# Kernel optimization log

Hardware: AMD Instinct MI355X
Metric: run time of the kernel (lower is better)

Reference implementation:

```python
import jax, jax.numpy as jnp
import numpy as np

N = 100000   # num nodes
E = 1600000  # num edges
F = 64       # node_feature_dim
H = 128      # hidden_dim
G = 64       # num graphs in batch
L = 3        # num_gnn_layers


def setup_inputs() -> dict:
    key = jax.random.key(0)
    ks = jax.random.split(key, 24)
    s = 0.05
    nrm = lambda k, shape: jax.random.normal(k, shape, jnp.float32) * s
    return dict(
        node_features=jax.random.normal(ks[0], (N, F), jnp.float32),
        edge_index=jax.random.randint(ks[1], (2, E), 0, N, dtype=jnp.int32),
        batch=jnp.sort(jax.random.randint(ks[2], (N,), 0, G, dtype=jnp.int32)),
        enc_w1=nrm(ks[3], (F, H)), enc_b1=jnp.zeros((H,), jnp.float32),
        enc_w2=nrm(ks[4], (H, H)), enc_b2=jnp.zeros((H,), jnp.float32),
        gcn_w=nrm(ks[5], (L, H, H)), gcn_b=jnp.zeros((L, H), jnp.float32),
        dec_w1=nrm(ks[6], (2 * H, H)), dec_b1=jnp.zeros((H,), jnp.float32),
        dec_w2=nrm(ks[7], (H, 64)), dec_b2=jnp.zeros((64,), jnp.float32),
        dec_w3=nrm(ks[8], (64, 3)), dec_b3=jnp.zeros((3,), jnp.float32),
        val_w1=nrm(ks[9], (2 * H, H)), val_b1=jnp.zeros((H,), jnp.float32),
        val_w2=nrm(ks[10], (H, 1)), val_b2=jnp.zeros((1,), jnp.float32),
    )


def _forward(node_features, edge_index, batch,
             enc_w1, enc_b1, enc_w2, enc_b2, gcn_w, gcn_b,
             dec_w1, dec_b1, dec_w2, dec_b2, dec_w3, dec_b3,
             val_w1, val_b1, val_w2, val_b2):
    n = node_features.shape[0]
    # node encoder (dropout is identity in eval)
    x = jax.nn.relu(node_features @ enc_w1 + enc_b1)
    x = x @ enc_w2 + enc_b2

    # GCN normalization with self-loops (PyG gcn_norm)
    loops = jnp.arange(n, dtype=edge_index.dtype)
    src = jnp.concatenate([edge_index[0], loops])
    dst = jnp.concatenate([edge_index[1], loops])
    deg = jax.ops.segment_sum(jnp.ones_like(src, jnp.float32), dst, num_segments=n)
    dinv = jax.lax.rsqrt(deg)  # deg >= 1 due to self-loops
    norm = (dinv[src] * dinv[dst])[:, None]  # [E+N, 1]

    for l in range(gcn_w.shape[0]):
        xw = x @ gcn_w[l]                      # [N, H]
        msg = xw[src] * norm                   # gather + scale
        agg = jax.ops.segment_sum(msg, dst, num_segments=n) + gcn_b[l]
        x = x + jax.nn.relu(agg)               # residual

    # global pools per graph
    graph_sum = jax.ops.segment_sum(x, batch, num_segments=G)
    counts = jax.ops.segment_sum(jnp.ones((n, 1), x.dtype), batch, num_segments=G)
    graph_mean = graph_sum / jnp.maximum(counts, 1.0)
    graph_max = jax.ops.segment_max(x, batch, num_segments=G)
    graph_repr = jnp.concatenate([graph_mean, graph_max], axis=1)  # [G, 2H]

    h = jax.nn.relu(graph_repr @ dec_w1 + dec_b1)
    h = jax.nn.relu(h @ dec_w2 + dec_b2)
    logits = h @ dec_w3 + dec_b3               # [G, 3]

    adaptation_prob = jax.nn.sigmoid(logits[:, 0])
    layer_priorities = jax.nn.softmax(logits[:, 1:2], axis=-1)
    urgency_score = jax.nn.sigmoid(logits[:, 2])

    v = jax.nn.relu(graph_repr @ val_w1 + val_b1)
    value_estimate = v @ val_w2 + val_b2       # [G, 1]
    return adaptation_prob, layer_priorities, urgency_score, value_estimate


def reference(node_features, edge_index, batch,
              enc_w1, enc_b1, enc_w2, enc_b2, gcn_w, gcn_b,
              dec_w1, dec_b1, dec_w2, dec_b2, dec_w3, dec_b3,
              val_w1, val_b1, val_w2, val_b2):
    return _forward(node_features, edge_index, batch,
                    enc_w1, enc_b1, enc_w2, enc_b2, gcn_w, gcn_b,
                    dec_w1, dec_b1, dec_w2, dec_b2, dec_w3, dec_b3,
                    val_w1, val_b1, val_w2, val_b2)
```

## Files before the change

kernel.cpp:

```cpp
#include <hip/hip_runtime.h>
#include <math.h>

constexpr int HD = 128;
constexpr int FD = 64;
constexpr int PCH = 32;
constexpr int BKT_SHIFT = 8;
constexpr int EPB = 8192;
constexpr float FP8_SCALE = 16.f;
constexpr float FP8_INV_SCALE = 1.f / 16.f;

typedef unsigned int uint;
typedef unsigned short ushort;
typedef unsigned char uchar;

using bf16x8 = __attribute__((ext_vector_type(8))) short;
using f32x4  = __attribute__((ext_vector_type(4))) float;

#if defined(__has_builtin)
#if __has_builtin(__builtin_amdgcn_cvt_pk_f32_fp8) && __has_builtin(__builtin_amdgcn_cvt_pk_fp8_f32)
#define HW_FP8 1
#endif
#endif

static __device__ inline ushort f2bf(float f) {
  uint u = __float_as_uint(f);
  return (ushort)((u + 0x7fffu + ((u >> 16) & 1u)) >> 16);
}
static __device__ inline float bf2f(ushort b) {
  return __uint_as_float((uint)b << 16);
}
static __device__ inline uint pack2bf(float a, float b) {
  return (uint)f2bf(a) | ((uint)f2bf(b) << 16);
}

static __device__ inline uchar enc_fp8_byte(float f) {
#ifdef HW_FP8
  return (uchar)(__builtin_amdgcn_cvt_pk_fp8_f32(f, f, 0, false) & 0xff);
#else
  float a = fabsf(f);
  uint s = (f < 0.f) ? 0x80u : 0u;
  if (!(a > 0.f)) return (uchar)s;
  a = fminf(a, 448.f);
  uint b = __float_as_uint(a);
  int e = (int)(b >> 23) - 127;
  if (e < -6) {
    int q = (int)rintf(a * 512.f);
    if (q <= 0) return (uchar)s;
    if (q >= 8) return (uchar)(s | 0x08u);
    return (uchar)(s | (uint)q);
  }
  uint r = b + 0x7ffffu + ((b >> 20) & 1u);
  uint m = (r >> 20) & 7u;
  int ee = (int)(r >> 23) - 127 + 7;
  if (ee <= 0) return (uchar)(s | 0x08u);
  if (ee > 15) return (uchar)(s | 0x7eu);
  return (uchar)(s | ((uint)ee << 3) | m);
#endif
}

static __device__ inline float dec_fp8_byte(uint em_s) {
  uint s = (em_s & 0x80u) << 24;
  uint em = em_s & 0x7fu;
  float v;
  if (em < 8) v = (float)em * (1.f / 512.f);
  else v = __uint_as_float((em + (120u << 3)) << 20);
  return __uint_as_float(__float_as_uint(v) | s);
}

static __device__ inline void dec_fp8x4(uint u, float* dst) {
#ifdef HW_FP8
  auto a = __builtin_amdgcn_cvt_pk_f32_fp8((int)u, false);
  auto b = __builtin_amdgcn_cvt_pk_f32_fp8((int)u, true);
  dst[0] = a[0]; dst[1] = a[1]; dst[2] = b[0]; dst[3] = b[1];
#else
  dst[0] = dec_fp8_byte(u & 0xffu);
  dst[1] = dec_fp8_byte((u >> 8) & 0xffu);
  dst[2] = dec_fp8_byte((u >> 16) & 0xffu);
  dst[3] = dec_fp8_byte(u >> 24);
#endif
}

__global__ void zero_int_kernel(int* __restrict__ p, int n) {
  int i = blockIdx.x * blockDim.x + threadIdx.x;
  if (i < n) p[i] = 0;
}

__global__ __launch_bounds__(256) void bucket_count_kernel(const int* __restrict__ dst,
    int* __restrict__ bucket_count, int e, int nbk) {
  __shared__ int hist[512];
  int t = threadIdx.x;
  for (int i = t; i < nbk; i += 256) hist[i] = 0;
  __syncthreads();
  int lo = blockIdx.x * EPB;
  int hi = lo + EPB; if (hi > e) hi = e;
  for (int i = lo + t; i < hi; i += 256) atomicAdd(&hist[dst[i] >> BKT_SHIFT], 1);
  __syncthreads();
  for (int i = t; i < nbk; i += 256) {
    int c = hist[i];
    if (c) atomicAdd(&bucket_count[i], c);
  }
}

__global__ __launch_bounds__(512) void bucket_scan_kernel(const int* __restrict__ bucket_count,
    int* __restrict__ bucket_base, int* __restrict__ bucket_cursor, int nbk) {
  __shared__ int sh[512];
  int t = threadIdx.x;
  int v = (t < nbk) ? bucket_count[t] : 0;
  sh[t] = v;
  __syncthreads();
  for (int d = 1; d < 512; d <<= 1) {
    int u = (t >= d) ? sh[t - d] : 0;
    __syncthreads();
    sh[t] += u;
    __syncthreads();
  }
  if (t < nbk) {
    int ex = sh[t] - v;
    bucket_base[t] = ex;
    bucket_cursor[t] = ex;
  }
  if (t == 511) bucket_base[nbk] = sh[511];
}

__global__ __launch_bounds__(256) void bucket_fill_kernel(const int* __restrict__ src,
    const int* __restrict__ dst, int* __restrict__ bucket_cursor,
    uint* __restrict__ pairs, int e, int nbk) {
  __shared__ int hist[512];
  int t = threadIdx.x;
  for (int i = t; i < nbk; i += 256) hist[i] = 0;
  __syncthreads();
  int lo = blockIdx.x * EPB;
  int hi = lo + EPB; if (hi > e) hi = e;
  for (int i = lo + t; i < hi; i += 256) atomicAdd(&hist[dst[i] >> BKT_SHIFT], 1);
  __syncthreads();
  for (int i = t; i < nbk; i += 256) {
    int c = hist[i];
    hist[i] = c ? atomicAdd(&bucket_cursor[i], c) : 0;
  }
  __syncthreads();
  for (int i = lo + t; i < hi; i += 256) {
    int s = src[i], d = dst[i];
    int pos = atomicAdd(&hist[d >> BKT_SHIFT], 1);
    pairs[pos] = ((uint)s << 8) | (uint)(d & 255);
  }
}

__global__ __launch_bounds__(256) void bucket_scatter_kernel(const uint* __restrict__ pairs,
    const int* __restrict__ bucket_base, int* __restrict__ offs,
    float* __restrict__ dinv, int* __restrict__ csr_src, int n, int nbk) {
  __shared__ int cnt[256];
  __shared__ int pre[256];
  int b = blockIdx.x, t = threadIdx.x;
  int node0 = b << BKT_SHIFT;
  bool valid_node = (node0 + t) < n;
  cnt[t] = 0;
  __syncthreads();
  int lo = bucket_base[b], hi = bucket_base[b + 1];
  for (int i = lo + t; i < hi; i += 256)
    atomicAdd(&cnt[pairs[i] & 255u], 1);
  __syncthreads();
  int v = cnt[t];
  pre[t] = v;
  __syncthreads();
  for (int d = 1; d < 256; d <<= 1) {
    int u = (t >= d) ? pre[t - d] : 0;
    __syncthreads();
    pre[t] += u;
    __syncthreads();
  }
  int off = lo + pre[t] - v;
  if (valid_node) {
    offs[node0 + t] = off;
    dinv[node0 + t] = rsqrtf((float)(v + 1));
  }
  __syncthreads();
  cnt[t] = off;
  __syncthreads();
  for (int i = lo + t; i < hi; i += 256) {
    uint pp = pairs[i];
    int pos = atomicAdd(&cnt[pp & 255u], 1);
    csr_src[pos] = (int)(pp >> 8);
  }
  if (b == 0 && t == 0) offs[n] = bucket_base[nbk];
}

__global__ void convert_wt_kernel(const float* __restrict__ W, ushort* __restrict__ wt,
                                  int KK) {
  int i = blockIdx.x * 256 + threadIdx.x;
  if (i < 128 * KK) {
    int c = i / KK, k = i - c * KK;
    wt[i] = f2bf(W[k * 128 + c]);
  }
}

template<typename TA, int K, bool BIAS, bool RELU, bool FP8OUT>
__global__ __launch_bounds__(256) void mfma_gemm_kernel(const TA* __restrict__ A,
    const ushort* __restrict__ Wt, const float* __restrict__ bias,
    void* __restrict__ Cout, const float* __restrict__ dinv, int M) {
  __shared__ ushort As[64 * K];
  __shared__ ushort Ws[128 * K];
  const int tid = threadIdx.x;
  const int r0 = blockIdx.x * 64;

  if constexpr (sizeof(TA) == 4) {
    constexpr int C4 = K / 4;
    const float4* A4 = (const float4*)A;
    #pragma unroll
    for (int i = tid; i < 64 * C4; i += 256) {
      int r = i / C4, c4 = i - r * C4;
      int row = r0 + r;
      float4 v = make_float4(0.f, 0.f, 0.f, 0.f);
      if (row < M) v = A4[(size_t)row * C4 + c4];
      ushort4 u;
      u.x = f2bf(v.x); u.y = f2bf(v.y); u.z = f2bf(v.z); u.w = f2bf(v.w);
      int elem = (r * K + c4 * 4) ^ ((r & 7) << 3);
      *(ushort4*)&As[elem] = u;
    }
  } else {
    constexpr int C8 = K / 8;
    const uint4* A4 = (const uint4*)A;
    #pragma unroll
    for (int i = tid; i < 64 * C8; i += 256) {
      int r = i / C8, c8 = i - r * C8;
      int row = r0 + r;
      uint4 v = make_uint4(0u, 0u, 0u, 0u);
      if (row < M) v = A4[(size_t)row * C8 + c8];
      int elem = (r * K + c8 * 8) ^ ((r & 7) << 3);
      *(uint4*)&As[elem] = v;
    }
  }
  {
    constexpr int C8 = K / 8;
    const uint4* W4 = (const uint4*)Wt;
    #pragma unroll
    for (int i = tid; i < 128 * C8; i += 256) {
      int c = i / C8, k8 = i - c * C8;
      uint4 v = W4[i];
      int elem = (c * K + k8 * 8) ^ ((c & 7) << 3);
      *(uint4*)&Ws[elem] = v;
    }
  }
  __syncthreads();

  const int l = tid & 63;
  const int wid = tid >> 6;
  const int lr = l & 15;
  const int lk = l >> 4;
  const int wr = wid * 16;
  f32x4 acc[8];
  #pragma unroll
  for (int cb = 0; cb < 8; ++cb) acc[cb] = (f32x4){0.f, 0.f, 0.f, 0.f};

  #pragma unroll
  for (int kc = 0; kc < K / 32; ++kc) {
    int ar = wr + lr;
    bf16x8 af = *(const bf16x8*)&As[(ar * K + kc * 32 + lk * 8) ^ ((ar & 7) << 3)];
    #pragma unroll
    for (int cb = 0; cb < 8; ++cb) {
      int col = cb * 16 + lr;
      bf16x8 bfr = *(const bf16x8*)&Ws[(col * K + kc * 32 + lk * 8) ^ ((col & 7) << 3)];
      acc[cb] = __builtin_amdgcn_mfma_f32_16x16x32_bf16(af, bfr, acc[cb], 0, 0, 0);
    }
  }

  if constexpr (FP8OUT) {
    uchar* C8p = (uchar*)Cout;
    float dv[4];
    #pragma unroll
    for (int j = 0; j < 4; ++j) {
      int row = r0 + wr + lk * 4 + j;
      dv[j] = (row < M) ? dinv[row] * FP8_SCALE : 0.f;
    }
    #pragma unroll
    for (int cb = 0; cb < 8; ++cb) {
      int col = cb * 16 + lr;
      #pragma unroll
      for (int j = 0; j < 4; ++j) {
        int row = r0 + wr + lk * 4 + j;
        if (row < M) {
          C8p[(size_t)row * 128 + col] = enc_fp8_byte(acc[cb][j] * dv[j]);
        }
      }
    }
  } else {
    ushort* Cb = (ushort*)Cout;
    #pragma unroll
    for (int cb = 0; cb < 8; ++cb) {
      int col = cb * 16 + lr;
      float bb = BIAS ? bias[col] : 0.f;
      #pragma unroll
      for (int j = 0; j < 4; ++j) {
        int row = r0 + wr + lk * 4 + j;
        if (row < M) {
          float o = acc[cb][j] + bb;
          if (RELU) o = fmaxf(o, 0.f);
          Cb[(size_t)row * 128 + col] = f2bf(o);
        }
      }
    }
  }
}

__global__ __launch_bounds__(256) void agg_update_kernel(
    const uchar* __restrict__ xws, ushort* __restrict__ x,
    const int* __restrict__ csr_src, const int* __restrict__ offs,
    const float* __restrict__ dinv, const float* __restrict__ bias, int n) {
  int node = blockIdx.x * 4 + (threadIdx.x >> 6);
  if (node >= n) return;
  int lane = threadIdx.x & 63;
  int grp = lane >> 4;
  int cl = lane & 15;
  const uint2* xw2 = (const uint2*)xws;
  float acc[8];
  #pragma unroll
  for (int k = 0; k < 8; ++k) acc[k] = 0.f;

  auto add_row = [&](uint2 v) {
    float f[4];
    dec_fp8x4(v.x, f);
    acc[0] += f[0]; acc[1] += f[1]; acc[2] += f[2]; acc[3] += f[3];
    dec_fp8x4(v.y, f);
    acc[4] += f[0]; acc[5] += f[1]; acc[6] += f[2]; acc[7] += f[3];
  };

  int beg = offs[node], end = offs[node + 1];
  int j = beg + grp;
  for (; j + 12 < end; j += 16) {
    int s0 = csr_src[j];
    int s1 = csr_src[j + 4];
    int s2 = csr_src[j + 8];
    int s3 = csr_src[j + 12];
    uint2 v0 = xw2[(size_t)s0 * 16 + cl];
    uint2 v1 = xw2[(size_t)s1 * 16 + cl];
    uint2 v2 = xw2[(size_t)s2 * 16 + cl];
    uint2 v3 = xw2[(size_t)s3 * 16 + cl];
    add_row(v0); add_row(v1); add_row(v2); add_row(v3);
  }
  for (; j + 4 < end; j += 8) {
    int s0 = csr_src[j];
    int s1 = csr_src[j + 4];
    uint2 v0 = xw2[(size_t)s0 * 16 + cl];
    uint2 v1 = xw2[(size_t)s1 * 16 + cl];
    add_row(v0); add_row(v1);
  }
  if (j < end) {
    uint2 v0 = xw2[(size_t)csr_src[j] * 16 + cl];
    add_row(v0);
  }
  if (grp == 0) {
    uint2 vi = xw2[(size_t)node * 16 + cl];
    add_row(vi);
  }
  #pragma unroll
  for (int k = 0; k < 8; ++k) {
    acc[k] += __shfl_xor(acc[k], 16);
    acc[k] += __shfl_xor(acc[k], 32);
  }
  if (grp == 0) {
    float di = dinv[node] * FP8_INV_SCALE;
    const float4* b4 = (const float4*)bias;
    float4 bb0 = b4[cl * 2], bb1 = b4[cl * 2 + 1];
    float bbv[8] = {bb0.x, bb0.y, bb0.z, bb0.w, bb1.x, bb1.y, bb1.z, bb1.w};
    uint4* xv4 = (uint4*)x;
    size_t xi = (size_t)node * 16 + cl;
    uint4 xv = xv4[xi];
    uint xu[4] = {xv.x, xv.y, xv.z, xv.w};
    float o[8];
    #pragma unroll
    for (int q = 0; q < 4; ++q) {
      float lo = __uint_as_float(xu[q] << 16);
      float hi = __uint_as_float(xu[q] & 0xffff0000u);
      o[2 * q]     = fmaxf(fmaf(acc[2 * q],     di, bbv[2 * q]),     0.f) + lo;
      o[2 * q + 1] = fmaxf(fmaf(acc[2 * q + 1], di, bbv[2 * q + 1]), 0.f) + hi;
    }
    uint4 ou;
    ou.x = pack2bf(o[0], o[1]);
    ou.y = pack2bf(o[2], o[3]);
    ou.z = pack2bf(o[4], o[5]);
    ou.w = pack2bf(o[6], o[7]);
    xv4[xi] = ou;
  }
}

__global__ void bounds_kernel(const int* __restrict__ batch, int* __restrict__ startg,
                              int n, int ng) {
  int i = blockIdx.x * blockDim.x + threadIdx.x;
  if (i > n) return;
  int bi = (i < n) ? batch[i] : ng;
  int bp = (i == 0) ? -1 : batch[i - 1];
  for (int g = bp + 1; g <= bi && g <= ng; ++g) startg[g] = i;
}

__global__ __launch_bounds__(256) void pool_partial_kernel(const ushort* __restrict__ x,
    const int* __restrict__ startg, float* __restrict__ psum, float* __restrict__ pmax) {
  __shared__ float ssum[16][128];
  __shared__ float smax[16][128];
  int g = blockIdx.x / PCH, ch = blockIdx.x % PCH;
  int t = threadIdx.x;
  int rg = t >> 4, cg = t & 15;
  int s0 = startg[g], s1 = startg[g + 1];
  int cnt = s1 - s0;
  int len = (cnt + PCH - 1) / PCH;
  int lo = s0 + ch * len;
  int hi = lo + len; if (hi > s1) hi = s1;
  float sum[8], mx[8];
  #pragma unroll
  for (int k = 0; k < 8; ++k) { sum[k] = 0.f; mx[k] = -INFINITY; }
  const uint4* x4 = (const uint4*)x;
  for (int r = lo + rg; r < hi; r += 16) {
    uint4 v = x4[(size_t)r * 16 + cg];
    uint uu[4] = {v.x, v.y, v.z, v.w};
    #pragma unroll
    for (int q = 0; q < 4; ++q) {
      float a = __uint_as_float(uu[q] << 16);
      float b = __uint_as_float(uu[q] & 0xffff0000u);
      sum[2 * q] += a;     mx[2 * q]     = fmaxf(mx[2 * q], a);
      sum[2 * q + 1] += b; mx[2 * q + 1] = fmaxf(mx[2 * q + 1], b);
    }
  }
  #pragma unroll
  for (int k = 0; k < 8; ++k) {
    ssum[rg][cg * 8 + k] = sum[k];
    smax[rg][cg * 8 + k] = mx[k];
  }
  __syncthreads();
  #pragma unroll
  for (int d = 8; d > 0; d >>= 1) {
    if (rg < d) {
      #pragma unroll
      for (int k = 0; k < 8; ++k) {
        int c = cg * 8 + k;
        ssum[rg][c] += ssum[rg + d][c];
        smax[rg][c] = fmaxf(smax[rg][c], smax[rg + d][c]);
      }
    }
    __syncthreads();
  }
  if (rg == 0) {
    #pragma unroll
    for (int k = 0; k < 8; ++k) {
      int c = cg * 8 + k;
      psum[(size_t)blockIdx.x * HD + c] = ssum[0][c];
      pmax[(size_t)blockIdx.x * HD + c] = smax[0][c];
    }
  }
}

__global__ __launch_bounds__(128) void pool_final_kernel(const float* __restrict__ psum,
    const float* __restrict__ pmax, const int* __restrict__ startg,
    float* __restrict__ repr) {
  int g = blockIdx.x, c = threadIdx.x;
  float sum = 0.f, mx = -INFINITY;
  #pragma unroll
  for (int ch = 0; ch < PCH; ++ch) {
    sum += psum[(size_t)(g * PCH + ch) * HD + c];
    mx = fmaxf(mx, pmax[(size_t)(g * PCH + ch) * HD + c]);
  }
  int cnt = startg[g + 1] - startg[g];
  float denom = (float)(cnt > 0 ? cnt : 1);
  repr[g * 256 + c] = sum / denom;
  repr[g * 256 + 128 + c] = mx;
}

__global__ __launch_bounds__(128) void heads_kernel(
    const float* __restrict__ repr,
    const float* __restrict__ dw1, const float* __restrict__ db1,
    const float* __restrict__ dw2, const float* __restrict__ db2,
    const float* __restrict__ dw3, const float* __restrict__ db3,
    const float* __restrict__ vw1, const float* __restrict__ vb1,
    const float* __restrict__ vw2, const float* __restrict__ vb2,
    float* __restrict__ out, int ng) {
  __shared__ float rep[256];
  __shared__ float h1[128];
  __shared__ float h2[64];
  __shared__ float v1[128];
  int g = blockIdx.x, t = threadIdx.x;
  rep[t] = repr[g * 256 + t];
  rep[128 + t] = repr[g * 256 + 128 + t];
  __syncthreads();
  float a = db1[t], b = vb1[t];
  for (int k = 0; k < 256; ++k) {
    float rv = rep[k];
    a = fmaf(rv, dw1[k * 128 + t], a);
    b = fmaf(rv, vw1[k * 128 + t], b);
  }
  h1[t] = fmaxf(a, 0.f);
  v1[t] = fmaxf(b, 0.f);
  __syncthreads();
  if (t < 64) {
    float c = db2[t];
    for (int k = 0; k < 128; ++k) c = fmaf(h1[k], dw2[k * 64 + t], c);
    h2[t] = fmaxf(c, 0.f);
  }
  __syncthreads();
  if (t == 0) {
    float l0 = db3[0], l2 = db3[2];
    for (int k = 0; k < 64; ++k) {
      l0 = fmaf(h2[k], dw3[k * 3 + 0], l0);
      l2 = fmaf(h2[k], dw3[k * 3 + 2], l2);
    }
    out[g] = 1.f / (1.f + expf(-l0));
    out[ng + g] = 1.0f;
    out[2 * ng + g] = 1.f / (1.f + expf(-l2));
    float v = vb2[0];
    for (int k = 0; k < 128; ++k) v = fmaf(v1[k], vw2[k], v);
    out[3 * ng + g] = v;
  }
}

extern "C" void kernel_launch(void* const* d_in, const int* in_sizes, int n_in,
                              void* d_out, int out_size, void* d_ws, size_t ws_size,
                              hipStream_t stream) {
  const float* nf     = (const float*)d_in[0];
  const int*   ei     = (const int*)d_in[1];
  const int*   batch  = (const int*)d_in[2];
  const float* enc_w1 = (const float*)d_in[3];
  const float* enc_b1 = (const float*)d_in[4];
  const float* enc_w2 = (const float*)d_in[5];
  const float* enc_b2 = (const float*)d_in[6];
  const float* gcn_w  = (const float*)d_in[7];
  const float* gcn_b  = (const float*)d_in[8];
  const float* dec_w1 = (const float*)d_in[9];
  const float* dec_b1 = (const float*)d_in[10];
  const float* dec_w2 = (const float*)d_in[11];
  const float* dec_b2 = (const float*)d_in[12];
  const float* dec_w3 = (const float*)d_in[13];
  const float* dec_b3 = (const float*)d_in[14];
  const float* val_w1 = (const float*)d_in[15];
  const float* val_b1 = (const float*)d_in[16];
  const float* val_w2 = (const float*)d_in[17];
  const float* val_b2 = (const float*)d_in[18];
  float* out = (float*)d_out;

  const int n = in_sizes[0] / FD;
  const int e = in_sizes[1] / 2;
  const int L = in_sizes[7] / (HD * HD);
  const int G = out_size / 4;

  char* p = (char*)d_ws;
  auto carve = [&](size_t bytes) {
    void* r = (void*)p;
    p += (bytes + 255) & ~(size_t)255;
    return r;
  };
  ushort* x       = (ushort*)carve((size_t)n * HD * 2);
  ushort* xwb     = (ushort*)carve((size_t)n * HD * 2);
  uchar*  xw8     = (uchar*)carve((size_t)n * HD);
  float*  dinv    = (float*)carve((size_t)n * 4);
  int*    offs    = (int*)carve((size_t)(n + 1) * 4);
  int*    csr_src = (int*)carve((size_t)e * 4);
  float*  repr    = (float*)carve((size_t)G * 256 * 4);
  int*    startg  = (int*)carve((size_t)(G + 1) * 4);
  float*  psum    = (float*)carve((size_t)G * PCH * HD * 4);
  float*  pmax    = (float*)carve((size_t)G * PCH * HD * 4);
  const int nbk   = (n + (1 << BKT_SHIFT) - 1) >> BKT_SHIFT;
  int*    bucket_count  = (int*)carve((size_t)nbk * 4);
  int*    bucket_base   = (int*)carve((size_t)(nbk + 1) * 4);
  int*    bucket_cursor = (int*)carve((size_t)nbk * 4);
  ushort* wt_e1   = (ushort*)carve((size_t)128 * FD * 2);
  ushort* wt_e2   = (ushort*)carve((size_t)128 * HD * 2);
  ushort* wt_g    = (ushort*)carve((size_t)3 * 128 * HD * 2);
  uint*   pairs   = (uint*)xwb;

  const int gemm_grid = (n + 63) / 64;
  const int ebk_grid = (e + EPB - 1) / EPB;

  zero_int_kernel<<<(nbk + 255) / 256, 256, 0, stream>>>(bucket_count, nbk);
  bucket_count_kernel<<<ebk_grid, 256, 0, stream>>>(ei + e, bucket_count, e, nbk);
  bucket_scan_kernel<<<1, 512, 0, stream>>>(bucket_count, bucket_base, bucket_cursor, nbk);
  bucket_fill_kernel<<<ebk_grid, 256, 0, stream>>>(ei, ei + e, bucket_cursor, pairs, e, nbk);
  bucket_scatter_kernel<<<nbk, 256, 0, stream>>>(pairs, bucket_base, offs, dinv, csr_src, n, nbk);

  convert_wt_kernel<<<(128 * FD + 255) / 256, 256, 0, stream>>>(enc_w1, wt_e1, FD);
  convert_wt_kernel<<<(128 * HD + 255) / 256, 256, 0, stream>>>(enc_w2, wt_e2, HD);
  for (int l = 0; l < L; ++l)
    convert_wt_kernel<<<(128 * HD + 255) / 256, 256, 0, stream>>>(
        gcn_w + (size_t)l * HD * HD, wt_g + (size_t)l * 128 * HD, HD);

  mfma_gemm_kernel<float, FD, true, true, false><<<gemm_grid, 256, 0, stream>>>(
      nf, wt_e1, enc_b1, xwb, nullptr, n);
  mfma_gemm_kernel<ushort, HD, true, false, false><<<gemm_grid, 256, 0, stream>>>(
      xwb, wt_e2, enc_b2, x, nullptr, n);

  for (int l = 0; l < L; ++l) {
    mfma_gemm_kernel<ushort, HD, false, false, true><<<gemm_grid, 256, 0, stream>>>(
        x, wt_g + (size_t)l * 128 * HD, nullptr, xw8, dinv, n);
    agg_update_kernel<<<(n + 3) / 4, 256, 0, stream>>>(
        xw8, x, csr_src, offs, dinv, gcn_b + (size_t)l * HD, n);
  }

  bounds_kernel<<<(n + 1 + 255) / 256, 256, 0, stream>>>(batch, startg, n, G);
  pool_partial_kernel<<<G * PCH, 256, 0, stream>>>(x, startg, psum, pmax);
  pool_final_kernel<<<G, 128, 0, stream>>>(psum, pmax, startg, repr);
  heads_kernel<<<G, 128, 0, stream>>>(repr,
      dec_w1, dec_b1, dec_w2, dec_b2, dec_w3, dec_b3,
      val_w1, val_b1, val_w2, val_b2, out, G);
}
```

Before: 372.8 us.

## Widen aggregation loads, fuse weight conversions and pool-final into heads, shrink EPB

The aggregation kernel now has each lane load 16 fp8 features (uint4) with 8 edge groups per wave instead of 4, which cuts per-edge load instructions but adds a third shuffle-reduction step and uses more accumulator registers. The five weight-conversion launches become a single kernel, and the pool-final reduction is folded into the heads kernel, removing launches and an intermediate buffer. The edges-per-block constant for the bucket kernels drops so that more blocks run. A leftover dead loop and scalar bias loads in the epilogue make that part untidy.

```diff
diff --git a/kernel.cpp b/kernel.cpp
--- a/kernel.cpp
+++ b/kernel.cpp
@@ -5,7 +5,7 @@
 constexpr int FD = 64;
 constexpr int PCH = 32;
 constexpr int BKT_SHIFT = 8;
-constexpr int EPB = 8192;
+constexpr int EPB = 2048;
 constexpr float FP8_SCALE = 16.f;
 constexpr float FP8_INV_SCALE = 1.f / 16.f;
 
@@ -184,12 +184,24 @@
   if (b == 0 && t == 0) offs[n] = bucket_base[nbk];
 }
 
-__global__ void convert_wt_kernel(const float* __restrict__ W, ushort* __restrict__ wt,
-                                  int KK) {
+__global__ void convert_all_wt_kernel(const float* __restrict__ enc_w1,
+    const float* __restrict__ enc_w2, const float* __restrict__ gcn_w,
+    ushort* __restrict__ wt_e1, ushort* __restrict__ wt_e2, ushort* __restrict__ wt_g,
+    int L) {
+  const int S0 = 128 * FD, S1 = 128 * HD;
   int i = blockIdx.x * 256 + threadIdx.x;
-  if (i < 128 * KK) {
-    int c = i / KK, k = i - c * KK;
-    wt[i] = f2bf(W[k * 128 + c]);
+  if (i < S0) {
+    int c = i / FD, k = i - c * FD;
+    wt_e1[i] = f2bf(enc_w1[k * 128 + c]);
+  } else if (i < S0 + S1) {
+    int j = i - S0;
+    int c = j / HD, k = j - c * HD;
+    wt_e2[j] = f2bf(enc_w2[k * 128 + c]);
+  } else if (i < S0 + S1 + L * S1) {
+    int j = i - S0 - S1;
+    int l = j / S1, jj = j - l * S1;
+    int c = jj / HD, k = jj - c * HD;
+    wt_g[(size_t)l * S1 + jj] = f2bf(gcn_w[(size_t)l * HD * HD + k * 128 + c]);
   }
 }
 
@@ -308,77 +320,84 @@
   int node = blockIdx.x * 4 + (threadIdx.x >> 6);
   if (node >= n) return;
   int lane = threadIdx.x & 63;
-  int grp = lane >> 4;
-  int cl = lane & 15;
-  const uint2* xw2 = (const uint2*)xws;
-  float acc[8];
+  int grp = lane >> 3;
+  int cl = lane & 7;
+  const uint4* xw4 = (const uint4*)xws;
+  float acc[16];
   #pragma unroll
-  for (int k = 0; k < 8; ++k) acc[k] = 0.f;
-
-  auto add_row = [&](uint2 v) {
+  for (int k = 0; k < 16; ++k) acc[k] = 0.f;
+
+  auto add_row = [&](uint4 v) {
     float f[4];
     dec_fp8x4(v.x, f);
     acc[0] += f[0]; acc[1] += f[1]; acc[2] += f[2]; acc[3] += f[3];
     dec_fp8x4(v.y, f);
     acc[4] += f[0]; acc[5] += f[1]; acc[6] += f[2]; acc[7] += f[3];
+    dec_fp8x4(v.z, f);
+    acc[8] += f[0]; acc[9] += f[1]; acc[10] += f[2]; acc[11] += f[3];
+    dec_fp8x4(v.w, f);
+    acc[12] += f[0]; acc[13] += f[1]; acc[14] += f[2]; acc[15] += f[3];
   };
 
   int beg = offs[node], end = offs[node + 1];
   int j = beg + grp;
-  for (; j + 12 < end; j += 16) {
+  for (; j + 8 < end; j += 16) {
     int s0 = csr_src[j];
-    int s1 = csr_src[j + 4];
-    int s2 = csr_src[j + 8];
-    int s3 = csr_src[j + 12];
-    uint2 v0 = xw2[(size_t)s0 * 16 + cl];
-    uint2 v1 = xw2[(size_t)s1 * 16 + cl];
-    uint2 v2 = xw2[(size_t)s2 * 16 + cl];
-    uint2 v3 = xw2[(size_t)s3 * 16 + cl];
-    add_row(v0); add_row(v1); add_row(v2); add_row(v3);
-  }
-  for (; j + 4 < end; j += 8) {
-    int s0 = csr_src[j];
-    int s1 = csr_src[j + 4];
-    uint2 v0 = xw2[(size_t)s0 * 16 + cl];
-    uint2 v1 = xw2[(size_t)s1 * 16 + cl];
+    int s1 = csr_src[j + 8];
+    uint4 v0 = xw4[(size_t)s0 * 8 + cl];
+    uint4 v1 = xw4[(size_t)s1 * 8 + cl];
     add_row(v0); add_row(v1);
   }
   if (j < end) {
-    uint2 v0 = xw2[(size_t)csr_src[j] * 16 + cl];
+    uint4 v0 = xw4[(size_t)csr_src[j] * 8 + cl];
     add_row(v0);
   }
   if (grp == 0) {
-    uint2 vi = xw2[(size_t)node * 16 + cl];
+    uint4 vi = xw4[(size_t)node * 8 + cl];
     add_row(vi);
   }
   #pragma unroll
-  for (int k = 0; k < 8; ++k) {
+  for (int k = 0; k < 16; ++k) {
+    acc[k] += __shfl_xor(acc[k], 8);
     acc[k] += __shfl_xor(acc[k], 16);
     acc[k] += __shfl_xor(acc[k], 32);
   }
   if (grp == 0) {
     float di = dinv[node] * FP8_INV_SCALE;
     const float4* b4 = (const float4*)bias;
-    float4 bb0 = b4[cl * 2], bb1 = b4[cl * 2 + 1];
-    float bbv[8] = {bb0.x, bb0.y, bb0.z, bb0.w, bb1.x, bb1.y, bb1.z, bb1.w};
     uint4* xv4 = (uint4*)x;
-    size_t xi = (size_t)node * 16 + cl;
-    uint4 xv = xv4[xi];
-    uint xu[4] = {xv.x, xv.y, xv.z, xv.w};
-    float o[8];
+    size_t xi = (size_t)node * 16 + cl * 2;
+    uint4 xa = xv4[xi], xb = xv4[xi + 1];
+    uint xu[8] = {xa.x, xa.y, xa.z, xa.w, xb.x, xb.y, xb.z, xb.w};
+    float o[16];
     #pragma unroll
     for (int q = 0; q < 4; ++q) {
-      float lo = __uint_as_float(xu[q] << 16);
-      float hi = __uint_as_float(xu[q] & 0xffff0000u);
-      o[2 * q]     = fmaxf(fmaf(acc[2 * q],     di, bbv[2 * q]),     0.f) + lo;
-      o[2 * q + 1] = fmaxf(fmaf(acc[2 * q + 1], di, bbv[2 * q + 1]), 0.f) + hi;
-    }
-    uint4 ou;
-    ou.x = pack2bf(o[0], o[1]);
-    ou.y = pack2bf(o[2], o[3]);
-    ou.z = pack2bf(o[4], o[5]);
-    ou.w = pack2bf(o[6], o[7]);
-    xv4[xi] = ou;
+      float4 bb = b4[cl * 4 + q];
+      float bv[4] = {bb.x, bb.y, bb.z, bb.w};
+      #pragma unroll
+      for (int r = 0; r < 2; ++r) {
+        int k = q * 4 + r * 2;
+        uint u = xu[q * 2 + r];
+      }
+    }
+    #pragma unroll
+    for (int d = 0; d < 16; d += 2) {
+      uint u = xu[d >> 1];
+      float lo = __uint_as_float(u << 16);
+      float hi = __uint_as_float(u & 0xffff0000u);
+      const float* bbp = (const float*)b4;
+      float b0 = bbp[16 * cl + d];
+      float b1 = bbp[16 * cl + d + 1];
+      o[d]     = fmaxf(fmaf(acc[d],     di, b0), 0.f) + lo;
+      o[d + 1] = fmaxf(fmaf(acc[d + 1], di, b1), 0.f) + hi;
+    }
+    uint4 oa, ob;
+    oa.x = pack2bf(o[0], o[1]);   oa.y = pack2bf(o[2], o[3]);
+    oa.z = pack2bf(o[4], o[5]);   oa.w = pack2bf(o[6], o[7]);
+    ob.x = pack2bf(o[8], o[9]);   ob.y = pack2bf(o[10], o[11]);
+    ob.z = pack2bf(o[12], o[13]); ob.w = pack2bf(o[14], o[15]);
+    xv4[xi] = oa;
+    xv4[xi + 1] = ob;
   }
 }
 
@@ -446,24 +465,9 @@
   }
 }
 
-__global__ __launch_bounds__(128) void pool_final_kernel(const float* __restrict__ psum,
-    const float* __restrict__ pmax, const int* __restrict__ startg,
-    float* __restrict__ repr) {
-  int g = blockIdx.x, c = threadIdx.x;
-  float sum = 0.f, mx = -INFINITY;
-  #pragma unroll
-  for (int ch = 0; ch < PCH; ++ch) {
-    sum += psum[(size_t)(g * PCH + ch) * HD + c];
-    mx = fmaxf(mx, pmax[(size_t)(g * PCH + ch) * HD + c]);
-  }
-  int cnt = startg[g + 1] - startg[g];
-  float denom = (float)(cnt > 0 ? cnt : 1);
-  repr[g * 256 + c] = sum / denom;
-  repr[g * 256 + 128 + c] = mx;
-}
-
 __global__ __launch_bounds__(128) void heads_kernel(
-    const float* __restrict__ repr,
+    const float* __restrict__ psum, const float* __restrict__ pmax,
+    const int* __restrict__ startg,
     const float* __restrict__ dw1, const float* __restrict__ db1,
     const float* __restrict__ dw2, const float* __restrict__ db2,
     const float* __restrict__ dw3, const float* __restrict__ db3,
@@ -475,8 +479,18 @@
   __shared__ float h2[64];
   __shared__ float v1[128];
   int g = blockIdx.x, t = threadIdx.x;
-  rep[t] = repr[g * 256 + t];
-  rep[128 + t] = repr[g * 256 + 128 + t];
+  {
+    float sum = 0.f, mx = -INFINITY;
+    #pragma unroll
+    for (int ch = 0; ch < PCH; ++ch) {
+      sum += psum[(size_t)(g * PCH + ch) * HD + t];
+      mx = fmaxf(mx, pmax[(size_t)(g * PCH + ch) * HD + t]);
+    }
+    int cnt = startg[g + 1] - startg[g];
+    float denom = (float)(cnt > 0 ? cnt : 1);
+    rep[t] = sum / denom;
+    rep[128 + t] = mx;
+  }
   __syncthreads();
   float a = db1[t], b = vb1[t];
   for (int k = 0; k < 256; ++k) {
@@ -549,7 +563,6 @@
   float*  dinv    = (float*)carve((size_t)n * 4);
   int*    offs    = (int*)carve((size_t)(n + 1) * 4);
   int*    csr_src = (int*)carve((size_t)e * 4);
-  float*  repr    = (float*)carve((size_t)G * 256 * 4);
   int*    startg  = (int*)carve((size_t)(G + 1) * 4);
   float*  psum    = (float*)carve((size_t)G * PCH * HD * 4);
   float*  pmax    = (float*)carve((size_t)G * PCH * HD * 4);
@@ -571,11 +584,11 @@
   bucket_fill_kernel<<<ebk_grid, 256, 0, stream>>>(ei, ei + e, bucket_cursor, pairs, e, nbk);
   bucket_scatter_kernel<<<nbk, 256, 0, stream>>>(pairs, bucket_base, offs, dinv, csr_src, n, nbk);
 
-  convert_wt_kernel<<<(128 * FD + 255) / 256, 256, 0, stream>>>(enc_w1, wt_e1, FD);
-  convert_wt_kernel<<<(128 * HD + 255) / 256, 256, 0, stream>>>(enc_w2, wt_e2, HD);
-  for (int l = 0; l < L; ++l)
-    convert_wt_kernel<<<(128 * HD + 255) / 256, 256, 0, stream>>>(
-        gcn_w + (size_t)l * HD * HD, wt_g + (size_t)l * 128 * HD, HD);
+  {
+    int tot = 128 * FD + 128 * HD + L * 128 * HD;
+    convert_all_wt_kernel<<<(tot + 255) / 256, 256, 0, stream>>>(
+        enc_w1, enc_w2, gcn_w, wt_e1, wt_e2, wt_g, L);
+  }
 
   mfma_gemm_kernel<float, FD, true, true, false><<<gemm_grid, 256, 0, stream>>>(
       nf, wt_e1, enc_b1, xwb, nullptr, n);
@@ -591,8 +604,7 @@
 
   bounds_kernel<<<(n + 1 + 255) / 256, 256, 0, stream>>>(batch, startg, n, G);
   pool_partial_kernel<<<G * PCH, 256, 0, stream>>>(x, startg, psum, pmax);
-  pool_final_kernel<<<G, 128, 0, stream>>>(psum, pmax, startg, repr);
-  heads_kernel<<<G, 128, 0, stream>>>(repr,
+  heads_kernel<<<G, 128, 0, stream>>>(psum, pmax, startg,
       dec_w1, dec_b1, dec_w2, dec_b2, dec_w3, dec_b3,
       val_w1, val_b1, val_w2, val_b2, out, G);
 }
```

New measurement: 396.0 us. 6.2% more time.

## Merge weight conversions and pool finalize into fewer launches; shrink edge block size

Applied to the files above, without the earlier changes.

The five per-matrix weight-conversion launches become a single kernel that indexes into all matrices. The pool-final reduction moves into the heads kernel, which drops one launch and the intermediate repr buffer. The edges-per-block constant for bucket count/fill drops from 8192 to 2048, giving more blocks for the edge bucketing kernels. The aim is less launch overhead and better parallelism in bucketing, at the cost of more atomic contention on the bucket counters.

```diff
diff --git a/kernel.cpp b/kernel.cpp
--- a/kernel.cpp
+++ b/kernel.cpp
@@ -5,7 +5,7 @@
 constexpr int FD = 64;
 constexpr int PCH = 32;
 constexpr int BKT_SHIFT = 8;
-constexpr int EPB = 8192;
+constexpr int EPB = 2048;
 constexpr float FP8_SCALE = 16.f;
 constexpr float FP8_INV_SCALE = 1.f / 16.f;
 
@@ -184,12 +184,24 @@
   if (b == 0 && t == 0) offs[n] = bucket_base[nbk];
 }
 
-__global__ void convert_wt_kernel(const float* __restrict__ W, ushort* __restrict__ wt,
-                                  int KK) {
+__global__ void convert_all_wt_kernel(const float* __restrict__ enc_w1,
+    const float* __restrict__ enc_w2, const float* __restrict__ gcn_w,
+    ushort* __restrict__ wt_e1, ushort* __restrict__ wt_e2, ushort* __restrict__ wt_g,
+    int L) {
+  const int S0 = 128 * FD, S1 = 128 * HD;
   int i = blockIdx.x * 256 + threadIdx.x;
-  if (i < 128 * KK) {
-    int c = i / KK, k = i - c * KK;
-    wt[i] = f2bf(W[k * 128 + c]);
+  if (i < S0) {
+    int c = i / FD, k = i - c * FD;
+    wt_e1[i] = f2bf(enc_w1[k * 128 + c]);
+  } else if (i < S0 + S1) {
+    int j = i - S0;
+    int c = j / HD, k = j - c * HD;
+    wt_e2[j] = f2bf(enc_w2[k * 128 + c]);
+  } else if (i < S0 + S1 + L * S1) {
+    int j = i - S0 - S1;
+    int l = j / S1, jj = j - l * S1;
+    int c = jj / HD, k = jj - c * HD;
+    wt_g[(size_t)l * S1 + jj] = f2bf(gcn_w[(size_t)l * HD * HD + k * 128 + c]);
   }
 }
 
@@ -446,24 +458,9 @@
   }
 }
 
-__global__ __launch_bounds__(128) void pool_final_kernel(const float* __restrict__ psum,
-    const float* __restrict__ pmax, const int* __restrict__ startg,
-    float* __restrict__ repr) {
-  int g = blockIdx.x, c = threadIdx.x;
-  float sum = 0.f, mx = -INFINITY;
-  #pragma unroll
-  for (int ch = 0; ch < PCH; ++ch) {
-    sum += psum[(size_t)(g * PCH + ch) * HD + c];
-    mx = fmaxf(mx, pmax[(size_t)(g * PCH + ch) * HD + c]);
-  }
-  int cnt = startg[g + 1] - startg[g];
-  float denom = (float)(cnt > 0 ? cnt : 1);
-  repr[g * 256 + c] = sum / denom;
-  repr[g * 256 + 128 + c] = mx;
-}
-
 __global__ __launch_bounds__(128) void heads_kernel(
-    const float* __restrict__ repr,
+    const float* __restrict__ psum, const float* __restrict__ pmax,
+    const int* __restrict__ startg,
     const float* __restrict__ dw1, const float* __restrict__ db1,
     const float* __restrict__ dw2, const float* __restrict__ db2,
     const float* __restrict__ dw3, const float* __restrict__ db3,
@@ -475,8 +472,18 @@
   __shared__ float h2[64];
   __shared__ float v1[128];
   int g = blockIdx.x, t = threadIdx.x;
-  rep[t] = repr[g * 256 + t];
-  rep[128 + t] = repr[g * 256 + 128 + t];
+  {
+    float sum = 0.f, mx = -INFINITY;
+    #pragma unroll
+    for (int ch = 0; ch < PCH; ++ch) {
+      sum += psum[(size_t)(g * PCH + ch) * HD + t];
+      mx = fmaxf(mx, pmax[(size_t)(g * PCH + ch) * HD + t]);
+    }
+    int cnt = startg[g + 1] - startg[g];
+    float denom = (float)(cnt > 0 ? cnt : 1);
+    rep[t] = sum / denom;
+    rep[128 + t] = mx;
+  }
   __syncthreads();
   float a = db1[t], b = vb1[t];
   for (int k = 0; k < 256; ++k) {
@@ -549,7 +556,6 @@
   float*  dinv    = (float*)carve((size_t)n * 4);
   int*    offs    = (int*)carve((size_t)(n + 1) * 4);
   int*    csr_src = (int*)carve((size_t)e * 4);
-  float*  repr    = (float*)carve((size_t)G * 256 * 4);
   int*    startg  = (int*)carve((size_t)(G + 1) * 4);
   float*  psum    = (float*)carve((size_t)G * PCH * HD * 4);
   float*  pmax    = (float*)carve((size_t)G * PCH * HD * 4);
@@ -571,11 +577,11 @@
   bucket_fill_kernel<<<ebk_grid, 256, 0, stream>>>(ei, ei + e, bucket_cursor, pairs, e, nbk);
   bucket_scatter_kernel<<<nbk, 256, 0, stream>>>(pairs, bucket_base, offs, dinv, csr_src, n, nbk);
 
-  convert_wt_kernel<<<(128 * FD + 255) / 256, 256, 0, stream>>>(enc_w1, wt_e1, FD);
-  convert_wt_kernel<<<(128 * HD + 255) / 256, 256, 0, stream>>>(enc_w2, wt_e2, HD);
-  for (int l = 0; l < L; ++l)
-    convert_wt_kernel<<<(128 * HD + 255) / 256, 256, 0, stream>>>(
-        gcn_w + (size_t)l * HD * HD, wt_g + (size_t)l * 128 * HD, HD);
+  {
+    int tot = 128 * FD + 128 * HD + L * 128 * HD;
+    convert_all_wt_kernel<<<(tot + 255) / 256, 256, 0, stream>>>(
+        enc_w1, enc_w2, gcn_w, wt_e1, wt_e2, wt_g, L);
+  }
 
   mfma_gemm_kernel<float, FD, true, true, false><<<gemm_grid, 256, 0, stream>>>(
       nf, wt_e1, enc_b1, xwb, nullptr, n);
@@ -591,8 +597,7 @@
 
   bounds_kernel<<<(n + 1 + 255) / 256, 256, 0, stream>>>(batch, startg, n, G);
   pool_partial_kernel<<<G * PCH, 256, 0, stream>>>(x, startg, psum, pmax);
-  pool_final_kernel<<<G, 128, 0, stream>>>(psum, pmax, startg, repr);
-  heads_kernel<<<G, 128, 0, stream>>>(repr,
+  heads_kernel<<<G, 128, 0, stream>>>(psum, pmax, startg,
       dec_w1, dec_b1, dec_w2, dec_b2, dec_w3, dec_b3,
       val_w1, val_b1, val_w2, val_b2, out, G);
 }
```

Measured after the change: 373.6 us. No clear change (+0.2%).
